# Kernel optimization log

Hardware: AMD Instinct MI355X
Metric: run time of the kernel (lower is better)

## Reference

```python
import jax, jax.numpy as jnp
import numpy as np

N_NODES = 65536
N_EDGES = 1048576
IN_FEATS = 128
H1 = 128
H2 = 256
N_CLASSES = 16


def setup_inputs() -> dict:
    key = jax.random.key(0)
    ks = jax.random.split(key, 12)
    s = 0.05
    x = jax.random.normal(ks[0], (N_NODES, IN_FEATS), dtype=jnp.float32)
    src = jax.random.randint(ks[1], (N_EDGES,), 0, N_NODES, dtype=jnp.int32)
    dst = jax.random.randint(ks[2], (N_EDGES,), 0, N_NODES, dtype=jnp.int32)
    # SAGEConv('pool') params: fc_pool (bias), fc_self (no bias), fc_neigh (no bias), output bias
    Wp = jax.random.normal(ks[3], (H1, IN_FEATS), dtype=jnp.float32) * s
    bp = jnp.zeros((H1,), dtype=jnp.float32)
    Ws = jax.random.normal(ks[4], (H1, IN_FEATS), dtype=jnp.float32) * s
    Wn = jax.random.normal(ks[5], (H1, H1), dtype=jnp.float32) * s
    bn = jnp.zeros((H1,), dtype=jnp.float32)
    # MLP head
    W1 = jax.random.normal(ks[6], (H2, H1), dtype=jnp.float32) * s
    b1 = jnp.zeros((H2,), dtype=jnp.float32)
    W2 = jax.random.normal(ks[7], (N_CLASSES, H2), dtype=jnp.float32) * s
    b2 = jnp.zeros((N_CLASSES,), dtype=jnp.float32)
    return {"x": x, "Wp": Wp, "bp": bp, "Ws": Ws, "Wn": Wn, "bn": bn,
            "W1": W1, "b1": b1, "W2": W2, "b2": b2, "src": src, "dst": dst}


def reference(x, Wp, bp, Ws, Wn, bn, W1, b1, W2, b2, src, dst):
    N = x.shape[0]
    # SAGEConv 'pool': per-edge MLP on gathered source features, segment-max over dst
    m = jax.nn.relu(x[src] @ Wp.T + bp)              # [E, H1]
    pooled = jax.ops.segment_max(m, dst, num_segments=N)  # [N, H1], -inf for isolated
    pooled = jnp.where(jnp.isneginf(pooled), 0.0, pooled)
    h = x @ Ws.T + pooled @ Wn.T + bn                # combine self + neigh
    h = jax.nn.leaky_relu(h)                         # slope 0.01 matches torch default
    h = jax.nn.leaky_relu(h @ W1.T + b1)
    # dropout is identity in eval mode
    h = jax.nn.sigmoid(h @ W2.T + b2)
    return h
```

## Files before the change

### kernel.cpp

```cpp
#include <hip/hip_runtime.h>
#include <cstdint>
#include <cstddef>

typedef __attribute__((ext_vector_type(8))) __bf16 bf16x8;
typedef __attribute__((ext_vector_type(4))) float f32x4;

union bf8pack { unsigned short u[8]; bf16x8 v; uint4 q; };

#define BCAP 768

static __device__ __forceinline__ unsigned short f2b(float f) {
    union { float f; unsigned int u; } v; v.f = f;
    unsigned int u = v.u;
    unsigned int r = (u + 0x7fffu + ((u >> 16) & 1u)) >> 16;
    return (unsigned short)r;
}

static __device__ __forceinline__ bf16x8 cvt8(const float* __restrict__ p) {
    float4 f0 = *(const float4*)p;
    float4 f1 = *(const float4*)(p + 4);
    bf8pack pk;
    pk.u[0] = f2b(f0.x); pk.u[1] = f2b(f0.y);
    pk.u[2] = f2b(f0.z); pk.u[3] = f2b(f0.w);
    pk.u[4] = f2b(f1.x); pk.u[5] = f2b(f1.y);
    pk.u[6] = f2b(f1.z); pk.u[7] = f2b(f1.w);
    return pk.v;
}

__global__ __launch_bounds__(256) void mega0(
    const int* __restrict__ src, const int* __restrict__ dst,
    int* __restrict__ bcnt, unsigned int* __restrict__ pairs,
    const float* __restrict__ x, const float* __restrict__ Wp,
    const float* __restrict__ bp,
    const float* __restrict__ Ws, const float* __restrict__ Wn,
    const float* __restrict__ W1, const float* __restrict__ W2,
    unsigned short* __restrict__ Wcat, unsigned short* __restrict__ W1_b,
    unsigned short* __restrict__ W2_b, unsigned short* __restrict__ y,
    unsigned short* __restrict__ xb)
{
    const int tid = threadIdx.x;
    const int bx = (int)blockIdx.x;

    if (bx >= 768) {
        int i = (bx - 768) * 256 + tid;
        if (i < 32768) {
            int o = i >> 8, k = i & 255;
            Wcat[i] = f2b(k < 128 ? Ws[o * 128 + k] : Wn[o * 128 + (k - 128)]);
        } else if (i < 65536) {
            W1_b[i - 32768] = f2b(W1[i - 32768]);
        } else {
            W2_b[i - 65536] = f2b(W2[i - 65536]);
        }
        return;
    }

    if (bx >= 256) {
        const int bm = bx - 256;
        const int w  = tid >> 6;
        const int wm = w & 1, wn = w >> 1;
        const int l  = tid & 63;
        const int lr = l & 15, quad = l >> 4;
        const int m0 = bm * 128 + wm * 64;
        const int n0 = wn * 64;

        f32x4 acc[4][4];
#pragma unroll
        for (int i = 0; i < 4; i++)
#pragma unroll
            for (int j = 0; j < 4; j++) acc[i][j] = (f32x4){0.f, 0.f, 0.f, 0.f};

        const float* Apf = x  + (size_t)(m0 + lr) * 128 + quad * 8;
        const float* Bpf = Wp + (size_t)(n0 + lr) * 128 + quad * 8;

#pragma unroll
        for (int ks = 0; ks < 4; ks++) {
            bf16x8 af[4], bf[4];
#pragma unroll
            for (int i = 0; i < 4; i++) {
                const float* p = Apf + (size_t)i * 16 * 128 + ks * 32;
                float4 f0 = *(const float4*)p;
                float4 f1 = *(const float4*)(p + 4);
                bf8pack pk;
                pk.u[0] = f2b(f0.x); pk.u[1] = f2b(f0.y);
                pk.u[2] = f2b(f0.z); pk.u[3] = f2b(f0.w);
                pk.u[4] = f2b(f1.x); pk.u[5] = f2b(f1.y);
                pk.u[6] = f2b(f1.z); pk.u[7] = f2b(f1.w);
                af[i] = pk.v;
                if (wn == 0)
                    *(uint4*)(xb + (size_t)(m0 + lr + i * 16) * 128 + ks * 32 + quad * 8) = pk.q;
            }
#pragma unroll
            for (int i = 0; i < 4; i++)
                bf[i] = cvt8(Bpf + (size_t)i * 16 * 128 + ks * 32);
#pragma unroll
            for (int mi = 0; mi < 4; mi++)
#pragma unroll
                for (int ni = 0; ni < 4; ni++)
                    acc[mi][ni] = __builtin_amdgcn_mfma_f32_16x16x32_bf16(
                        af[mi], bf[ni], acc[mi][ni], 0, 0, 0);
        }

#pragma unroll
        for (int ni = 0; ni < 4; ni++) {
            const int col = n0 + ni * 16 + lr;
            const float bv = bp[col];
#pragma unroll
            for (int mi = 0; mi < 4; mi++) {
#pragma unroll
                for (int r = 0; r < 4; r++) {
                    const int row = m0 + mi * 16 + quad * 4 + r;
                    float v = acc[mi][ni][r] + bv;
                    v = v > 0.f ? v : 0.f;
                    y[(size_t)row * 128 + col] = f2b(v);
                }
            }
        }
        return;
    }

    __shared__ int h[2048];
    __shared__ int base_l[2048];
    __shared__ int cnt[2048];
    for (int i = tid; i < 2048; i += 256) { h[i] = 0; cnt[i] = 0; }
    __syncthreads();
    const int base = bx * 4096;
    int d_r[16], s_r[16];
    const int4* s4 = (const int4*)(src + base);
    const int4* d4 = (const int4*)(dst + base);
#pragma unroll
    for (int i = 0; i < 4; i++) {
        int4 dv = d4[tid + i * 256];
        int4 sv = s4[tid + i * 256];
        d_r[i * 4 + 0] = dv.x; d_r[i * 4 + 1] = dv.y;
        d_r[i * 4 + 2] = dv.z; d_r[i * 4 + 3] = dv.w;
        s_r[i * 4 + 0] = sv.x; s_r[i * 4 + 1] = sv.y;
        s_r[i * 4 + 2] = sv.z; s_r[i * 4 + 3] = sv.w;
    }
#pragma unroll
    for (int i = 0; i < 16; i++)
        atomicAdd(&h[((unsigned)d_r[i]) >> 5], 1);
    __syncthreads();
    for (int i = tid; i < 2048; i += 256)
        base_l[i] = h[i] ? (i * BCAP + atomicAdd(&bcnt[i], h[i])) : 0;
    __syncthreads();
#pragma unroll
    for (int i = 0; i < 16; i++) {
        int b = ((unsigned)d_r[i]) >> 5;
        int pos = base_l[b] + atomicAdd(&cnt[b], 1);
        if (pos < (b + 1) * BCAP)
            pairs[pos] = ((unsigned)s_r[i] << 5) | ((unsigned)d_r[i] & 31u);
    }
}

__global__ __launch_bounds__(256, 4) void megaB(
    const unsigned int* __restrict__ yu, const int* __restrict__ bcnt,
    const unsigned int* __restrict__ pairs,
    const unsigned short* __restrict__ xb,
    const unsigned short* __restrict__ Wcat, const float* __restrict__ bn,
    const unsigned short* __restrict__ W1_b, const float* __restrict__ b1,
    const unsigned short* __restrict__ W2_b, const float* __restrict__ b2,
    float* __restrict__ out)
{
    __shared__ unsigned short S[32 * 264];
    __shared__ unsigned short ldsSrc[1024];
    __shared__ int bin[32], offl[32], cnt2[32];
    unsigned int* PS = (unsigned int*)&S[32 * 136];

    const int b = blockIdx.x;
    const int tid = threadIdx.x;
    const int w = tid >> 6, l = tid & 63;
    const int lr = l & 15, quad = l >> 4;
    const int row0 = b * 32;

    if (tid < 32) { bin[tid] = 0; cnt2[tid] = 0; }
    __syncthreads();
    const int beg = b * BCAP;
    int nb = bcnt[b]; nb = nb < BCAP ? nb : BCAP;

    for (int i = tid; i < nb; i += 256)
        atomicAdd(&bin[pairs[beg + i] & 31u], 1);
    __syncthreads();
    if (tid == 0) {
        int run = 0;
        for (int i = 0; i < 32; i++) { offl[i] = run; run += bin[i]; }
    }
    __syncthreads();
    for (int i = tid; i < nb; i += 256) {
        unsigned int p = pairs[beg + i];
        int d = p & 31u;
        int slot = offl[d] + atomicAdd(&cnt2[d], 1);
        ldsSrc[slot] = (unsigned short)(p >> 5);
    }
    __syncthreads();

    for (int ni = 0; ni < 8; ni++) {
        const int n = w * 8 + ni;
        const int e0 = offl[n], cnt = bin[n];
        float ax = 0.f, ay = 0.f;
        for (int e = 0; e < cnt; e += 8) {
            int s[8]; unsigned int v[8];
#pragma unroll
            for (int j = 0; j < 8; j++) {
                int idx = e + j; idx = idx < cnt ? idx : cnt - 1;
                s[j] = ldsSrc[e0 + idx];
            }
#pragma unroll
            for (int j = 0; j < 8; j++) v[j] = yu[(size_t)s[j] * 64 + l];
#pragma unroll
            for (int j = 0; j < 8; j++) {
                ax = fmaxf(ax, __uint_as_float(v[j] << 16));
                ay = fmaxf(ay, __uint_as_float(v[j] & 0xffff0000u));
            }
        }
        unsigned int packed = (__float_as_uint(ax) >> 16) | (__float_as_uint(ay) & 0xffff0000u);
        PS[n * 64 + (l ^ ((n & 7) << 2))] = packed;
    }
    __syncthreads();

    {
        f32x4 acc[2][2];
#pragma unroll
        for (int i = 0; i < 2; i++)
#pragma unroll
            for (int j = 0; j < 2; j++) acc[i][j] = (f32x4){0.f, 0.f, 0.f, 0.f};

        const unsigned short* Axp = xb + (size_t)(row0 + lr) * 128 + quad * 8;
        const unsigned short* Bp = Wcat + (size_t)(w * 32 + lr) * 256 + quad * 8;

#pragma unroll
        for (int ks = 0; ks < 8; ks++) {
            bf16x8 af[2], bf[2];
            if (ks < 4) {
#pragma unroll
                for (int i = 0; i < 2; i++)
                    af[i] = *(const bf16x8*)(Axp + (size_t)i * 16 * 128 + ks * 32);
            } else {
#pragma unroll
                for (int i = 0; i < 2; i++) {
                    const int row = i * 16 + lr;
                    const int c0 = (ks - 4) * 16 + quad * 4;
                    af[i] = *(const bf16x8*)&PS[row * 64 + (c0 ^ ((row & 7) << 2))];
                }
            }
#pragma unroll
            for (int i = 0; i < 2; i++)
                bf[i] = *(const bf16x8*)(Bp + (size_t)i * 16 * 256 + ks * 32);
#pragma unroll
            for (int mi = 0; mi < 2; mi++)
#pragma unroll
                for (int ni = 0; ni < 2; ni++)
                    acc[mi][ni] = __builtin_amdgcn_mfma_f32_16x16x32_bf16(
                        af[mi], bf[ni], acc[mi][ni], 0, 0, 0);
        }

#pragma unroll
        for (int ni = 0; ni < 2; ni++) {
            const int col = w * 32 + ni * 16 + lr;
            const float bv = bn[col];
#pragma unroll
            for (int mi = 0; mi < 2; mi++) {
#pragma unroll
                for (int r = 0; r < 4; r++) {
                    const int row = mi * 16 + quad * 4 + r;
                    float v = acc[mi][ni][r] + bv;
                    v = v > 0.f ? v : 0.01f * v;
                    S[row * 136 + col] = f2b(v);
                }
            }
        }
    }
    __syncthreads();

    {
        f32x4 acc[2][4];
#pragma unroll
        for (int i = 0; i < 2; i++)
#pragma unroll
            for (int j = 0; j < 4; j++) acc[i][j] = (f32x4){0.f, 0.f, 0.f, 0.f};

        const unsigned short* Bp = W1_b + (size_t)(w * 64 + lr) * 128 + quad * 8;

#pragma unroll
        for (int ks = 0; ks < 4; ks++) {
            bf16x8 af[2], bfr[4];
#pragma unroll
            for (int i = 0; i < 2; i++)
                af[i] = *(const bf16x8*)&S[(i * 16 + lr) * 136 + ks * 32 + quad * 8];
#pragma unroll
            for (int i = 0; i < 4; i++)
                bfr[i] = *(const bf16x8*)(Bp + (size_t)i * 16 * 128 + ks * 32);
#pragma unroll
            for (int mi = 0; mi < 2; mi++)
#pragma unroll
                for (int ni = 0; ni < 4; ni++)
                    acc[mi][ni] = __builtin_amdgcn_mfma_f32_16x16x32_bf16(
                        af[mi], bfr[ni], acc[mi][ni], 0, 0, 0);
        }
        __syncthreads();

#pragma unroll
        for (int ni = 0; ni < 4; ni++) {
            const int col = w * 64 + ni * 16 + lr;
            const float bv = b1[col];
#pragma unroll
            for (int mi = 0; mi < 2; mi++) {
#pragma unroll
                for (int r = 0; r < 4; r++) {
                    const int row = mi * 16 + quad * 4 + r;
                    float v = acc[mi][ni][r] + bv;
                    v = v > 0.f ? v : 0.01f * v;
                    S[row * 264 + col] = f2b(v);
                }
            }
        }
    }
    __syncthreads();

    if (w < 2) {
        const int m0 = w * 16;
        f32x4 a2 = (f32x4){0.f, 0.f, 0.f, 0.f};
#pragma unroll
        for (int ks = 0; ks < 8; ks++) {
            bf16x8 a = *(const bf16x8*)&S[(m0 + lr) * 264 + ks * 32 + quad * 8];
            bf16x8 bb = *(const bf16x8*)(W2_b + (size_t)lr * 256 + ks * 32 + quad * 8);
            a2 = __builtin_amdgcn_mfma_f32_16x16x32_bf16(a, bb, a2, 0, 0, 0);
        }
        const float bv = b2[lr];
#pragma unroll
        for (int r = 0; r < 4; r++) {
            const int row = row0 + m0 + quad * 4 + r;
            float v = a2[r] + bv;
            out[(size_t)row * 16 + lr] = 1.f / (1.f + __expf(-v));
        }
    }
}

extern "C" void kernel_launch(void* const* d_in, const int* in_sizes, int n_in,
                              void* d_out, int out_size, void* d_ws, size_t ws_size,
                              hipStream_t stream)
{
    const float* x  = (const float*)d_in[0];
    const float* Wp = (const float*)d_in[1];
    const float* bp = (const float*)d_in[2];
    const float* Ws = (const float*)d_in[3];
    const float* Wn = (const float*)d_in[4];
    const float* bn = (const float*)d_in[5];
    const float* W1 = (const float*)d_in[6];
    const float* b1 = (const float*)d_in[7];
    const float* W2 = (const float*)d_in[8];
    const float* b2 = (const float*)d_in[9];
    const int* src  = (const int*)d_in[10];
    const int* dst  = (const int*)d_in[11];
    float* out = (float*)d_out;

    const int N = in_sizes[0] / 128;

    unsigned short* y    = (unsigned short*)d_ws;
    unsigned short* xb   = (unsigned short*)((char*)d_ws + (size_t)16 * 1024 * 1024);
    unsigned short* Wcat = (unsigned short*)((char*)d_ws + (size_t)32 * 1024 * 1024);
    unsigned short* W1_b = Wcat + 32768;
    unsigned short* W2_b = W1_b + 32768;
    int* bcnt = (int*)(W2_b + 4096);
    unsigned int* pairs = (unsigned int*)(bcnt + 2048);

    dim3 blk(256);

    hipMemsetAsync(bcnt, 0, 2048 * sizeof(int), stream);

    mega0<<<1040, blk, 0, stream>>>(src, dst, bcnt, pairs,
                                    x, Wp, bp, Ws, Wn, W1, W2,
                                    Wcat, W1_b, W2_b, y, xb);

    megaB<<<N / 32, blk, 0, stream>>>((const unsigned int*)y, bcnt, pairs,
                                      xb, Wcat, bn, W1_b, b1, W2_b, b2, out);
}
```

Baseline: 206.2 us.

## Batch gather of four nodes per wave with packed u16 max and padded edge lists

Replaces the serial single-thread prefix sum over bins with a wave shuffle scan, and pads each destination's edge list to a multiple of 8 by repeating the last source. The segment-max loop now processes four destination nodes at once per wave, loading 8 source indices with one vector LDS read and issuing up to 32 independent gathers per iteration. This raises memory-level parallelism. The bf16 max uses v_pk_max_u16 on the raw bits, which is only valid because the values are post-ReLU and non-negative. Padding increases the LDS footprint per bin, which could overflow the ldsSrc buffer when counts are near capacity.

After: 205.4 us. No clear change (-0.4%).

```diff
diff --git a/kernel.cpp b/kernel.cpp
--- a/kernel.cpp
+++ b/kernel.cpp
@@ -25,6 +25,12 @@
     pk.u[4] = f2b(f1.x); pk.u[5] = f2b(f1.y);
     pk.u[6] = f2b(f1.z); pk.u[7] = f2b(f1.w);
     return pk.v;
+}
+
+static __device__ __forceinline__ unsigned int pkmax(unsigned int a, unsigned int b) {
+    unsigned int d;
+    asm("v_pk_max_u16 %0, %1, %2" : "=v"(d) : "v"(a), "v"(b));
+    return d;
 }
 
 __global__ __launch_bounds__(256) void mega0(
@@ -180,11 +186,20 @@
     for (int i = tid; i < nb; i += 256)
         atomicAdd(&bin[pairs[beg + i] & 31u], 1);
     __syncthreads();
-    if (tid == 0) {
-        int run = 0;
-        for (int i = 0; i < 32; i++) { offl[i] = run; run += bin[i]; }
-    }
-    __syncthreads();
+
+    if (tid < 32) {
+        int c = bin[tid];
+        int p = (c + 7) & ~7;
+        int s = p;
+#pragma unroll
+        for (int d = 1; d < 32; d <<= 1) {
+            int t = __shfl_up(s, d);
+            if (tid >= d) s += t;
+        }
+        offl[tid] = s - p;
+    }
+    __syncthreads();
+
     for (int i = tid; i < nb; i += 256) {
         unsigned int p = pairs[beg + i];
         int d = p & 31u;
@@ -193,27 +208,64 @@
     }
     __syncthreads();
 
-    for (int ni = 0; ni < 8; ni++) {
-        const int n = w * 8 + ni;
-        const int e0 = offl[n], cnt = bin[n];
-        float ax = 0.f, ay = 0.f;
-        for (int e = 0; e < cnt; e += 8) {
-            int s[8]; unsigned int v[8];
-#pragma unroll
-            for (int j = 0; j < 8; j++) {
-                int idx = e + j; idx = idx < cnt ? idx : cnt - 1;
-                s[j] = ldsSrc[e0 + idx];
-            }
-#pragma unroll
-            for (int j = 0; j < 8; j++) v[j] = yu[(size_t)s[j] * 64 + l];
-#pragma unroll
-            for (int j = 0; j < 8; j++) {
-                ax = fmaxf(ax, __uint_as_float(v[j] << 16));
-                ay = fmaxf(ay, __uint_as_float(v[j] & 0xffff0000u));
-            }
-        }
-        unsigned int packed = (__float_as_uint(ax) >> 16) | (__float_as_uint(ay) & 0xffff0000u);
-        PS[n * 64 + (l ^ ((n & 7) << 2))] = packed;
+    if (tid < 32) {
+        int c = bin[tid];
+        if (c > 0) {
+            int o = offl[tid];
+            unsigned short last = ldsSrc[o + c - 1];
+            int p = (c + 7) & ~7;
+            for (int k = c; k < p; k++) ldsSrc[o + k] = last;
+        }
+    }
+    __syncthreads();
+
+    const unsigned int* __restrict__ ylane = yu + l;
+#pragma unroll
+    for (int g = 0; g < 2; g++) {
+        const int n0 = w * 8 + g * 4;
+        unsigned int acc[4] = {0u, 0u, 0u, 0u};
+        int e0a[4], rka[4];
+#pragma unroll
+        for (int k = 0; k < 4; k++) {
+            e0a[k] = offl[n0 + k];
+            rka[k] = (bin[n0 + k] + 7) >> 3;
+        }
+        int maxr = rka[0];
+#pragma unroll
+        for (int k = 1; k < 4; k++) maxr = rka[k] > maxr ? rka[k] : maxr;
+
+        for (int r = 0; r < maxr; r++) {
+            unsigned int vv[4][8];
+#pragma unroll
+            for (int k = 0; k < 4; k++) {
+                if (r < rka[k]) {
+                    uint4 sv = *(const uint4*)&ldsSrc[e0a[k] + r * 8];
+                    vv[k][0] = ylane[(size_t)(sv.x & 0xffffu) << 6];
+                    vv[k][1] = ylane[(size_t)(sv.x >> 16) << 6];
+                    vv[k][2] = ylane[(size_t)(sv.y & 0xffffu) << 6];
+                    vv[k][3] = ylane[(size_t)(sv.y >> 16) << 6];
+                    vv[k][4] = ylane[(size_t)(sv.z & 0xffffu) << 6];
+                    vv[k][5] = ylane[(size_t)(sv.z >> 16) << 6];
+                    vv[k][6] = ylane[(size_t)(sv.w & 0xffffu) << 6];
+                    vv[k][7] = ylane[(size_t)(sv.w >> 16) << 6];
+                }
+            }
+#pragma unroll
+            for (int k = 0; k < 4; k++) {
+                if (r < rka[k]) {
+                    unsigned int m01 = pkmax(vv[k][0], vv[k][1]);
+                    unsigned int m23 = pkmax(vv[k][2], vv[k][3]);
+                    unsigned int m45 = pkmax(vv[k][4], vv[k][5]);
+                    unsigned int m67 = pkmax(vv[k][6], vv[k][7]);
+                    acc[k] = pkmax(acc[k], pkmax(pkmax(m01, m23), pkmax(m45, m67)));
+                }
+            }
+        }
+#pragma unroll
+        for (int k = 0; k < 4; k++) {
+            const int n = n0 + k;
+            PS[n * 64 + (l ^ ((n & 7) << 2))] = acc[k];
+        }
     }
     __syncthreads();
 
```
